# Kernel tuning notes

Hardware: AMD Instinct MI355X
Metric: run time of the kernel (lower is better)

The kernel has to match this reference:

```python
import jax, jax.numpy as jnp
import numpy as np

D_MODEL = 1024
N_HEADS = 16
HEAD = D_MODEL // N_HEADS
SEQ_THRESHOLD = 2048
EPS = 1e-12  # torch F.normalize eps


def setup_inputs() -> dict:
    key = jax.random.key(0)
    ks = jax.random.split(key, 12)
    B, L = 2, 2048
    s = 1.0 / np.sqrt(D_MODEL)
    inp = {
        "query": jax.random.normal(ks[0], (B, L, D_MODEL), jnp.float32),
        "key": jax.random.normal(ks[1], (B, L, D_MODEL), jnp.float32),
        "value": jax.random.normal(ks[2], (B, L, D_MODEL), jnp.float32),
        "mask": jnp.ones((B, 1, 1, L), jnp.int32),
        "Wq": jax.random.normal(ks[3], (D_MODEL, D_MODEL), jnp.float32) * s,
        "bq": jnp.zeros((D_MODEL,), jnp.float32),
        "Wk": jax.random.normal(ks[4], (D_MODEL, D_MODEL), jnp.float32) * s,
        "bk": jnp.zeros((D_MODEL,), jnp.float32),
        "Wv": jax.random.normal(ks[5], (D_MODEL, D_MODEL), jnp.float32) * s,
        "bv": jnp.zeros((D_MODEL,), jnp.float32),
        "Wo": jax.random.normal(ks[6], (D_MODEL, D_MODEL), jnp.float32) * s,
        "bo": jnp.zeros((D_MODEL,), jnp.float32),
        "scale": jnp.asarray(np.log2(SEQ_THRESHOLD**2 - SEQ_THRESHOLD), jnp.float32),
    }
    return inp


def _split_heads(x):  # [B,L,D] -> [B,H,L,hd]
    B, L, _ = x.shape
    return x.reshape(B, L, N_HEADS, HEAD).transpose(0, 2, 1, 3)


def _l2norm(x):
    n = jnp.sqrt(jnp.sum(x * x, axis=-1, keepdims=True))
    return x / jnp.maximum(n, EPS)


def reference(query, key, value, mask, Wq, bq, Wk, bk, Wv, bv, Wo, bo, scale):
    Q = _split_heads(query @ Wq.T + bq)
    K = _split_heads(key @ Wk.T + bk)
    V = _split_heads(value @ Wv.T + bv)
    Q = _l2norm(Q)
    K = _l2norm(K)
    # scaled cosine attention scores [B,H,Lq,Lk]
    scores = scale * jnp.einsum("bhqd,bhkd->bhqk", Q, K)
    scores = jnp.where(mask == 0, jnp.float32(-1e18), scores)
    attn = jax.nn.softmax(scores, axis=-1)
    ctx = jnp.einsum("bhqk,bhkd->bhqd", attn, V)
    B, H, Lq, hd = ctx.shape
    ctx = ctx.transpose(0, 2, 1, 3).reshape(B, Lq, H * hd)
    out = ctx @ Wo.T + bo
    return (out, attn)
```

## Files before the change

### kernel.cpp

```cpp
#include <hip/hip_runtime.h>
#include <hip/hip_bf16.h>
#include <stdint.h>

typedef __attribute__((ext_vector_type(8))) short bf16x8;
typedef __attribute__((ext_vector_type(4))) float f32x4;

#define LSEQ 2048
#define DM 1024
#define NH 16
#define HD 64

__device__ __forceinline__ unsigned short bf16r(float f) {
  unsigned u = __builtin_bit_cast(unsigned, f);
  u = (u + 0x7FFFu + ((u >> 16) & 1u)) >> 16;
  return (unsigned short)u;
}
__device__ __forceinline__ float bf16f(unsigned short h) {
  unsigned u = ((unsigned)h) << 16;
  return __builtin_bit_cast(float, u);
}

__device__ __forceinline__ void async16(const void* g, void* l) {
  __builtin_amdgcn_global_load_lds(
      (const __attribute__((address_space(1))) unsigned int*)g,
      (__attribute__((address_space(3))) unsigned int*)l, 16, 0, 0);
}

template <int ROWB>
__device__ __forceinline__ bf16x8 lds_frag_swz(const unsigned short* base, int row, int colbyte) {
  int addr = row * ROWB + colbyte;
  addr ^= ((row & 7) << 4);
  return *(const bf16x8*)((const char*)base + addr);
}
__device__ __forceinline__ void lds_store16_swz(unsigned short* base, int row, int col,
                                                unsigned short v) {
  int addr = row * 256 + col * 2;
  addr ^= ((row & 7) << 4);
  *(unsigned short*)((char*)base + addr) = v;
}

__global__ __launch_bounds__(256) void cvt3(const float* __restrict__ s0,
                                            const float* __restrict__ s1,
                                            const float* __restrict__ s2,
                                            unsigned short* __restrict__ d0,
                                            unsigned short* __restrict__ d1,
                                            unsigned short* __restrict__ d2, int n8) {
  int y = blockIdx.y;
  const float* s = (y == 0) ? s0 : (y == 1) ? s1 : s2;
  unsigned short* d = (y == 0) ? d0 : (y == 1) ? d1 : d2;
  int i = blockIdx.x * 256 + threadIdx.x;
  if (i >= n8) return;
  const float4* sp = (const float4*)s;
  float4 a = sp[2 * i], b = sp[2 * i + 1];
  union { unsigned short u[8]; uint4 v; } r;
  r.u[0] = bf16r(a.x); r.u[1] = bf16r(a.y); r.u[2] = bf16r(a.z); r.u[3] = bf16r(a.w);
  r.u[4] = bf16r(b.x); r.u[5] = bf16r(b.y); r.u[6] = bf16r(b.z); r.u[7] = bf16r(b.w);
  ((uint4*)d)[i] = r.v;
}
__global__ __launch_bounds__(256) void cvt4(const float* __restrict__ s0,
                                            const float* __restrict__ s1,
                                            const float* __restrict__ s2,
                                            const float* __restrict__ s3,
                                            unsigned short* __restrict__ d0,
                                            unsigned short* __restrict__ d1,
                                            unsigned short* __restrict__ d2,
                                            unsigned short* __restrict__ d3, int n8) {
  int y = blockIdx.y;
  const float* s = (y == 0) ? s0 : (y == 1) ? s1 : (y == 2) ? s2 : s3;
  unsigned short* d = (y == 0) ? d0 : (y == 1) ? d1 : (y == 2) ? d2 : d3;
  int i = blockIdx.x * 256 + threadIdx.x;
  if (i >= n8) return;
  const float4* sp = (const float4*)s;
  float4 a = sp[2 * i], b = sp[2 * i + 1];
  union { unsigned short u[8]; uint4 v; } r;
  r.u[0] = bf16r(a.x); r.u[1] = bf16r(a.y); r.u[2] = bf16r(a.z); r.u[3] = bf16r(a.w);
  r.u[4] = bf16r(b.x); r.u[5] = bf16r(b.y); r.u[6] = bf16r(b.z); r.u[7] = bf16r(b.w);
  ((uint4*)d)[i] = r.v;
}

__device__ __forceinline__ void gemm_core(const unsigned short* __restrict__ A,
                                          const unsigned short* __restrict__ Bw,
                                          const float* __restrict__ bias,
                                          void* __restrict__ Cout, int mode,
                                          unsigned short* As, unsigned short* Bs) {
  const int t = threadIdx.x, lane = t & 63, wid = t >> 6;
  const int mt = blockIdx.x, nt = blockIdx.y;
  const int wm = (wid >> 1) * 64, wn = (wid & 1) * 64;
  const int lq = lane >> 4, lr = lane & 15;

  f32x4 acc[4][4];
#pragma unroll
  for (int i = 0; i < 4; ++i)
#pragma unroll
    for (int j = 0; j < 4; ++j) acc[i][j] = (f32x4){0.f, 0.f, 0.f, 0.f};

  auto stage = [&](int k0) {
#pragma unroll
    for (int i = 0; i < 4; ++i) {
      int chunk = i * 256 + t;
      int row = chunk >> 3, j = chunk & 7;
      int sj = j ^ (row & 7);
      async16(A + (size_t)(mt * 128 + row) * DM + k0 + sj * 8, (char*)As + chunk * 16);
    }
#pragma unroll
    for (int i = 0; i < 4; ++i) {
      int chunk = i * 256 + t;
      int row = chunk >> 3, j = chunk & 7;
      int sj = j ^ (row & 7);
      async16(Bw + (size_t)(nt * 128 + row) * DM + k0 + sj * 8, (char*)Bs + chunk * 16);
    }
  };

  stage(0);
  for (int kt = 0; kt < DM / 64; ++kt) {
    __syncthreads();
    bf16x8 af[4][2], bfr[4][2];
#pragma unroll
    for (int mf = 0; mf < 4; ++mf) {
      int row = wm + mf * 16 + lr;
#pragma unroll
      for (int ks = 0; ks < 2; ++ks)
        af[mf][ks] = lds_frag_swz<128>(As, row, ks * 64 + lq * 16);
    }
#pragma unroll
    for (int nf = 0; nf < 4; ++nf) {
      int row = wn + nf * 16 + lr;
#pragma unroll
      for (int ks = 0; ks < 2; ++ks)
        bfr[nf][ks] = lds_frag_swz<128>(Bs, row, ks * 64 + lq * 16);
    }
    __syncthreads();
    if (kt + 1 < DM / 64) stage((kt + 1) * 64);
#pragma unroll
    for (int ks = 0; ks < 2; ++ks)
#pragma unroll
      for (int mf = 0; mf < 4; ++mf)
#pragma unroll
        for (int nf = 0; nf < 4; ++nf)
          acc[mf][nf] = __builtin_amdgcn_mfma_f32_16x16x32_bf16(af[mf][ks], bfr[nf][ks],
                                                                acc[mf][nf], 0, 0, 0);
  }

  const int gn0 = nt * 128 + wn;
  float bv[4];
#pragma unroll
  for (int nf = 0; nf < 4; ++nf) bv[nf] = bias[gn0 + nf * 16 + lr];
#pragma unroll
  for (int mf = 0; mf < 4; ++mf) {
    float v[4][4];
#pragma unroll
    for (int nf = 0; nf < 4; ++nf)
#pragma unroll
      for (int r = 0; r < 4; ++r) v[nf][r] = acc[mf][nf][r] + bv[nf];
    if (mode == 1) {
#pragma unroll
      for (int r = 0; r < 4; ++r) {
        float ss = v[0][r] * v[0][r] + v[1][r] * v[1][r] + v[2][r] * v[2][r] + v[3][r] * v[3][r];
        ss += __shfl_xor(ss, 1, 64);
        ss += __shfl_xor(ss, 2, 64);
        ss += __shfl_xor(ss, 4, 64);
        ss += __shfl_xor(ss, 8, 64);
        float rn = 1.0f / fmaxf(sqrtf(ss), 1e-12f);
#pragma unroll
        for (int nf = 0; nf < 4; ++nf) v[nf][r] *= rn;
      }
    }
    const int gm0 = mt * 128 + wm + mf * 16 + lq * 4;
    if (mode == 2) {
      float* C = (float*)Cout;
#pragma unroll
      for (int r = 0; r < 4; ++r)
#pragma unroll
        for (int nf = 0; nf < 4; ++nf)
          C[(size_t)(gm0 + r) * DM + gn0 + nf * 16 + lr] = v[nf][r];
    } else {
      unsigned short* C = (unsigned short*)Cout;
#pragma unroll
      for (int r = 0; r < 4; ++r)
#pragma unroll
        for (int nf = 0; nf < 4; ++nf)
          C[(size_t)(gm0 + r) * DM + gn0 + nf * 16 + lr] = bf16r(v[nf][r]);
    }
  }
}

__global__ __launch_bounds__(256) void gemm_qkv(
    const unsigned short* __restrict__ A0, const unsigned short* __restrict__ A1,
    const unsigned short* __restrict__ A2, const unsigned short* __restrict__ W0,
    const unsigned short* __restrict__ W1, const unsigned short* __restrict__ W2,
    const float* __restrict__ b0, const float* __restrict__ b1, const float* __restrict__ b2,
    unsigned short* __restrict__ C0, unsigned short* __restrict__ C1,
    unsigned short* __restrict__ C2) {
  __shared__ unsigned short As[128 * 64];
  __shared__ unsigned short Bs[128 * 64];
  int z = blockIdx.z;
  const unsigned short* A = (z == 0) ? A0 : (z == 1) ? A1 : A2;
  const unsigned short* W = (z == 0) ? W0 : (z == 1) ? W1 : W2;
  const float* bias = (z == 0) ? b0 : (z == 1) ? b1 : b2;
  unsigned short* C = (z == 0) ? C0 : (z == 1) ? C1 : C2;
  gemm_core(A, W, bias, C, (z == 2) ? 0 : 1, As, Bs);
}

__global__ __launch_bounds__(256) void gemm_o(const unsigned short* __restrict__ A,
                                              const unsigned short* __restrict__ W,
                                              const float* __restrict__ bias,
                                              float* __restrict__ C) {
  __shared__ unsigned short As[128 * 64];
  __shared__ unsigned short Bs[128 * 64];
  gemm_core(A, W, bias, C, 2, As, Bs);
}

__global__ __launch_bounds__(256) void transpose_v(const unsigned short* __restrict__ V,
                                                   unsigned short* __restrict__ Vt) {
  __shared__ unsigned short T[64][72];
  const int lt = blockIdx.x, h = blockIdx.y, b = blockIdx.z;
  const int t = threadIdx.x;
  const int r = t >> 2, c0 = (t & 3) * 16;
  const unsigned short* g = V + ((size_t)(b * LSEQ + lt * 64 + r) * DM + h * 64 + c0);
  *(uint4*)&T[r][c0] = *(const uint4*)g;
  *(uint4*)&T[r][c0 + 8] = *(const uint4*)(g + 8);
  __syncthreads();
  const int d = t >> 2, l0 = (t & 3) * 16;
  union { unsigned short u[16]; uint4 v[2]; } o;
#pragma unroll
  for (int j = 0; j < 16; ++j) o.u[j] = T[l0 + j][d];
  unsigned short* og = Vt + ((size_t)((b * NH + h) * HD + d) * LSEQ + lt * 64 + l0);
  ((uint4*)og)[0] = o.v[0];
  ((uint4*)og)[1] = o.v[1];
}

__global__ __launch_bounds__(256) void attn_kernel(
    const unsigned short* __restrict__ Qn, const unsigned short* __restrict__ Kn,
    const unsigned short* __restrict__ Vt, const int* __restrict__ mask,
    const float* __restrict__ scale_p, float* __restrict__ attn_out,
    unsigned short* __restrict__ ctx) {
  __shared__ unsigned short PQs[64 * 128];
  __shared__ unsigned short Ks[128 * 64];
  __shared__ unsigned short Vs[64 * 128];
  const int qt = blockIdx.x, h = blockIdx.y, b = blockIdx.z;
  const int t = threadIdx.x, lane = t & 63, wid = t >> 6;
  const int lq = lane >> 4, lr = lane & 15;
  const int wq = wid * 16;
  const float k2 = scale_p[0] * 1.4426950408889634f;

  const unsigned short* Qg = Qn + ((size_t)(b * LSEQ + qt * 64) * DM + h * HD);
  const unsigned short* Kg = Kn + ((size_t)b * LSEQ * DM + h * HD);
  const unsigned short* Vg = Vt + (size_t)(b * NH + h) * HD * LSEQ;
  float* attn_g = attn_out + ((size_t)((b * NH + h) * LSEQ + qt * 64)) * LSEQ;
  const int* mg = mask + b * LSEQ;

  auto stageK = [&](int k0) {
#pragma unroll
    for (int i = 0; i < 4; ++i) {
      int chunk = i * 256 + t;
      int row = chunk >> 3, j = chunk & 7;
      async16(Kg + (size_t)(k0 + row) * DM + (j ^ (row & 7)) * 8, (char*)Ks + chunk * 16);
    }
  };
  auto stageV = [&](int k0) {
#pragma unroll
    for (int i = 0; i < 4; ++i) {
      int chunk = i * 256 + t;
      int row = chunk >> 4, j = chunk & 15;
      async16(Vg + (size_t)row * LSEQ + k0 + (j ^ (row & 7)) * 8, (char*)Vs + chunk * 16);
    }
  };

#pragma unroll
  for (int i = 0; i < 2; ++i) {
    int chunk = i * 256 + t;
    int row = chunk >> 3, j = chunk & 7;
    async16(Qg + (size_t)row * DM + (j ^ (row & 7)) * 8, (char*)PQs + chunk * 16);
  }
  stageK(0);

  bf16x8 qa[2];
  float rsum[4] = {0.f, 0.f, 0.f, 0.f};

  auto qk_tile = [&](f32x4 (&c)[8]) {
#pragma unroll
    for (int nf = 0; nf < 8; ++nf) {
      int row = nf * 16 + lr;
      bf16x8 k0f = lds_frag_swz<128>(Ks, row, lq * 16);
      bf16x8 k1f = lds_frag_swz<128>(Ks, row, 64 + lq * 16);
      f32x4 z = (f32x4){0.f, 0.f, 0.f, 0.f};
      z = __builtin_amdgcn_mfma_f32_16x16x32_bf16(qa[0], k0f, z, 0, 0, 0);
      z = __builtin_amdgcn_mfma_f32_16x16x32_bf16(qa[1], k1f, z, 0, 0, 0);
      c[nf] = z;
    }
  };

  for (int kt = 0; kt < LSEQ / 128; ++kt) {
    __syncthreads();
    if (kt == 0) {
      int row = wq + lr;
      qa[0] = lds_frag_swz<128>(PQs, row, lq * 16);
      qa[1] = lds_frag_swz<128>(PQs, row, 64 + lq * 16);
    }
    f32x4 c[8];
    qk_tile(c);
    __syncthreads();
    if (kt + 1 < LSEQ / 128) stageK((kt + 1) * 128);
#pragma unroll
    for (int nf = 0; nf < 8; ++nf) {
      int mv = mg[kt * 128 + nf * 16 + lr];
#pragma unroll
      for (int r = 0; r < 4; ++r) {
        float p = exp2f(c[nf][r] * k2);
        rsum[r] += mv ? p : 0.f;
      }
    }
  }
  stageK(0);
  stageV(0);
#pragma unroll
  for (int off = 1; off < 16; off <<= 1)
#pragma unroll
    for (int r = 0; r < 4; ++r) rsum[r] += __shfl_xor(rsum[r], off, 64);
  float sinv[4];
#pragma unroll
  for (int r = 0; r < 4; ++r) sinv[r] = 1.0f / fmaxf(rsum[r], 1e-30f);

  f32x4 opv[4];
#pragma unroll
  for (int nf = 0; nf < 4; ++nf) opv[nf] = (f32x4){0.f, 0.f, 0.f, 0.f};
  unsigned short* Ps = PQs;
  for (int kt = 0; kt < LSEQ / 128; ++kt) {
    __syncthreads();
    f32x4 c[8];
    qk_tile(c);
#pragma unroll
    for (int nf = 0; nf < 8; ++nf) {
      int mv = mg[kt * 128 + nf * 16 + lr];
#pragma unroll
      for (int r = 0; r < 4; ++r) {
        float p = mv ? exp2f(c[nf][r] * k2) * sinv[r] : 0.f;
        lds_store16_swz(Ps, wq + lq * 4 + r, nf * 16 + lr, bf16r(p));
      }
    }
    __syncthreads();
    if (kt + 1 < LSEQ / 128) stageK((kt + 1) * 128);
    {
      int rr = t >> 4, c8 = (t & 15) * 8;
      float* og = attn_g + kt * 128 + c8;
#pragma unroll
      for (int gi = 0; gi < 4; ++gi) {
        int row = gi * 16 + rr;
        bf16x8 p8 = lds_frag_swz<256>(Ps, row, c8 * 2);
        f32x4 f0, f1;
        f0[0] = bf16f((unsigned short)p8[0]); f0[1] = bf16f((unsigned short)p8[1]);
        f0[2] = bf16f((unsigned short)p8[2]); f0[3] = bf16f((unsigned short)p8[3]);
        f1[0] = bf16f((unsigned short)p8[4]); f1[1] = bf16f((unsigned short)p8[5]);
        f1[2] = bf16f((unsigned short)p8[6]); f1[3] = bf16f((unsigned short)p8[7]);
        float* rp = og + (size_t)row * LSEQ;
        __builtin_nontemporal_store(f0, (f32x4*)rp);
        __builtin_nontemporal_store(f1, (f32x4*)(rp + 4));
      }
    }
#pragma unroll
    for (int ks = 0; ks < 4; ++ks) {
      bf16x8 pa = lds_frag_swz<256>(Ps, wq + lr, ks * 64 + lq * 16);
#pragma unroll
      for (int nf = 0; nf < 4; ++nf) {
        bf16x8 vb = lds_frag_swz<256>(Vs, nf * 16 + lr, ks * 64 + lq * 16);
        opv[nf] = __builtin_amdgcn_mfma_f32_16x16x32_bf16(pa, vb, opv[nf], 0, 0, 0);
      }
    }
    __syncthreads();
    if (kt + 1 < LSEQ / 128) stageV((kt + 1) * 128);
  }
#pragma unroll
  for (int nf = 0; nf < 4; ++nf)
#pragma unroll
    for (int r = 0; r < 4; ++r) {
      int q = wq + lq * 4 + r;
      int d = nf * 16 + lr;
      ctx[(size_t)(b * LSEQ + qt * 64 + q) * DM + h * HD + d] = bf16r(opv[nf][r]);
    }
}

extern "C" void kernel_launch(void* const* d_in, const int* in_sizes, int n_in,
                              void* d_out, int out_size, void* d_ws, size_t ws_size,
                              hipStream_t stream) {
  const float* query = (const float*)d_in[0];
  const float* key_ = (const float*)d_in[1];
  const float* value = (const float*)d_in[2];
  const int* mask = (const int*)d_in[3];
  const float* Wq = (const float*)d_in[4];
  const float* bq = (const float*)d_in[5];
  const float* Wk = (const float*)d_in[6];
  const float* bk = (const float*)d_in[7];
  const float* Wv = (const float*)d_in[8];
  const float* bv = (const float*)d_in[9];
  const float* Wo = (const float*)d_in[10];
  const float* bo = (const float*)d_in[11];
  const float* scale = (const float*)d_in[12];

  char* ws = (char*)d_ws;
  const size_t XB = 8388608;
  const size_t WB = 2097152;
  unsigned short* qb = (unsigned short*)(ws);
  unsigned short* kb = (unsigned short*)(ws + XB);
  unsigned short* vb = (unsigned short*)(ws + 2 * XB);
  unsigned short* wqb = (unsigned short*)(ws + 3 * XB);
  unsigned short* wkb = (unsigned short*)(ws + 3 * XB + WB);
  unsigned short* wvb = (unsigned short*)(ws + 3 * XB + 2 * WB);
  unsigned short* wob = (unsigned short*)(ws + 3 * XB + 3 * WB);
  unsigned short* Qnb = (unsigned short*)(ws + 3 * XB + 4 * WB);
  unsigned short* Knb = (unsigned short*)(ws + 4 * XB + 4 * WB);
  unsigned short* Vb = (unsigned short*)(ws + 5 * XB + 4 * WB);
  unsigned short* Vtb = (unsigned short*)(ws + 6 * XB + 4 * WB);
  unsigned short* ctxb = (unsigned short*)(ws + 7 * XB + 4 * WB);

  cvt3<<<dim3(2048, 3), 256, 0, stream>>>(query, key_, value, qb, kb, vb, 524288);
  cvt4<<<dim3(512, 4), 256, 0, stream>>>(Wq, Wk, Wv, Wo, wqb, wkb, wvb, wob, 131072);

  gemm_qkv<<<dim3(32, 8, 3), 256, 0, stream>>>(qb, kb, vb, wqb, wkb, wvb, bq, bk, bv,
                                               Qnb, Knb, Vb);
  transpose_v<<<dim3(32, NH, 2), 256, 0, stream>>>(Vb, Vtb);

  float* attn_out = (float*)d_out + 4194304;
  attn_kernel<<<dim3(32, NH, 2), 256, 0, stream>>>(Qnb, Knb, Vtb, mask, scale, attn_out, ctxb);

  gemm_o<<<dim3(32, 8), 256, 0, stream>>>(ctxb, wob, bo, (float*)d_out);
}
```

Baseline: 291.6 us.

## Fuse V transpose into QKV GEMM and keep attention probabilities in registers

The V projection GEMM now writes its output directly in transposed per-head layout, which removes the separate transpose kernel and its buffer. The attention kernel computes S^T with swapped MFMA operands. Probabilities are stored to the attn output straight from registers and packed to bf16 with v_cvt_pk_bf16, then redistributed through cross-lane shuffles into the PV MFMA operand, so the LDS round-trip for P is gone. The mask is preloaded to LDS as bf16 multipliers, the K/V staging sync is merged, and launch bounds allow 4 blocks per CU. The costs are extra shuffle instructions and strided 8-byte stores in the V epilogue.

```diff
diff --git a/kernel.cpp b/kernel.cpp
--- a/kernel.cpp
+++ b/kernel.cpp
@@ -19,6 +19,11 @@
   unsigned u = ((unsigned)h) << 16;
   return __builtin_bit_cast(float, u);
 }
+__device__ __forceinline__ unsigned cvt_pk_bf16(float a, float b) {
+  unsigned r;
+  asm("v_cvt_pk_bf16_f32 %0, %1, %2" : "=v"(r) : "v"(a), "v"(b));
+  return r;
+}
 
 __device__ __forceinline__ void async16(const void* g, void* l) {
   __builtin_amdgcn_global_load_lds(
@@ -26,17 +31,15 @@
       (__attribute__((address_space(3))) unsigned int*)l, 16, 0, 0);
 }
 
-template <int ROWB>
 __device__ __forceinline__ bf16x8 lds_frag_swz(const unsigned short* base, int row, int colbyte) {
-  int addr = row * ROWB + colbyte;
+  int addr = row * 128 + colbyte;
   addr ^= ((row & 7) << 4);
   return *(const bf16x8*)((const char*)base + addr);
 }
-__device__ __forceinline__ void lds_store16_swz(unsigned short* base, int row, int col,
-                                                unsigned short v) {
-  int addr = row * 256 + col * 2;
-  addr ^= ((row & 7) << 4);
-  *(unsigned short*)((char*)base + addr) = v;
+__device__ __forceinline__ bf16x8 lds_frag_swzV(const unsigned short* base, int row, int colbyte) {
+  int addr = row * 256 + colbyte;
+  addr ^= ((row & 15) << 4);
+  return *(const bf16x8*)((const char*)base + addr);
 }
 
 __global__ __launch_bounds__(256) void cvt3(const float* __restrict__ s0,
@@ -78,10 +81,11 @@
   ((uint4*)d)[i] = r.v;
 }
 
+template <int MODE>
 __device__ __forceinline__ void gemm_core(const unsigned short* __restrict__ A,
                                           const unsigned short* __restrict__ Bw,
                                           const float* __restrict__ bias,
-                                          void* __restrict__ Cout, int mode,
+                                          void* __restrict__ Cout,
                                           unsigned short* As, unsigned short* Bs) {
   const int t = threadIdx.x, lane = t & 63, wid = t >> 6;
   const int mt = blockIdx.x, nt = blockIdx.y;
@@ -120,14 +124,14 @@
       int row = wm + mf * 16 + lr;
 #pragma unroll
       for (int ks = 0; ks < 2; ++ks)
-        af[mf][ks] = lds_frag_swz<128>(As, row, ks * 64 + lq * 16);
+        af[mf][ks] = lds_frag_swz(As, row, ks * 64 + lq * 16);
     }
 #pragma unroll
     for (int nf = 0; nf < 4; ++nf) {
       int row = wn + nf * 16 + lr;
 #pragma unroll
       for (int ks = 0; ks < 2; ++ks)
-        bfr[nf][ks] = lds_frag_swz<128>(Bs, row, ks * 64 + lq * 16);
+        bfr[nf][ks] = lds_frag_swz(Bs, row, ks * 64 + lq * 16);
     }
     __syncthreads();
     if (kt + 1 < DM / 64) stage((kt + 1) * 64);
@@ -152,7 +156,7 @@
     for (int nf = 0; nf < 4; ++nf)
 #pragma unroll
       for (int r = 0; r < 4; ++r) v[nf][r] = acc[mf][nf][r] + bv[nf];
-    if (mode == 1) {
+    if (MODE == 1) {
 #pragma unroll
       for (int r = 0; r < 4; ++r) {
         float ss = v[0][r] * v[0][r] + v[1][r] * v[1][r] + v[2][r] * v[2][r] + v[3][r] * v[3][r];
@@ -166,13 +170,25 @@
       }
     }
     const int gm0 = mt * 128 + wm + mf * 16 + lq * 4;
-    if (mode == 2) {
+    if (MODE == 2) {
       float* C = (float*)Cout;
 #pragma unroll
       for (int r = 0; r < 4; ++r)
 #pragma unroll
         for (int nf = 0; nf < 4; ++nf)
           C[(size_t)(gm0 + r) * DM + gn0 + nf * 16 + lr] = v[nf][r];
+    } else if (MODE == 3) {
+      unsigned short* Vt = (unsigned short*)Cout;
+      const int bb = gm0 >> 11, ll = gm0 & 2047;
+#pragma unroll
+      for (int nf = 0; nf < 4; ++nf) {
+        int col = gn0 + nf * 16 + lr;
+        int hh = col >> 6, dd = col & 63;
+        ushort4 o;
+        o.x = bf16r(v[nf][0]); o.y = bf16r(v[nf][1]);
+        o.z = bf16r(v[nf][2]); o.w = bf16r(v[nf][3]);
+        *(ushort4*)&Vt[(size_t)((bb * NH + hh) * HD + dd) * LSEQ + ll] = o;
+      }
     } else {
       unsigned short* C = (unsigned short*)Cout;
 #pragma unroll
@@ -194,11 +210,9 @@
   __shared__ unsigned short As[128 * 64];
   __shared__ unsigned short Bs[128 * 64];
   int z = blockIdx.z;
-  const unsigned short* A = (z == 0) ? A0 : (z == 1) ? A1 : A2;
-  const unsigned short* W = (z == 0) ? W0 : (z == 1) ? W1 : W2;
-  const float* bias = (z == 0) ? b0 : (z == 1) ? b1 : b2;
-  unsigned short* C = (z == 0) ? C0 : (z == 1) ? C1 : C2;
-  gemm_core(A, W, bias, C, (z == 2) ? 0 : 1, As, Bs);
+  if (z == 0) gemm_core<1>(A0, W0, b0, C0, As, Bs);
+  else if (z == 1) gemm_core<1>(A1, W1, b1, C1, As, Bs);
+  else gemm_core<3>(A2, W2, b2, C2, As, Bs);
 }
 
 __global__ __launch_bounds__(256) void gemm_o(const unsigned short* __restrict__ A,
@@ -207,36 +221,17 @@
                                               float* __restrict__ C) {
   __shared__ unsigned short As[128 * 64];
   __shared__ unsigned short Bs[128 * 64];
-  gemm_core(A, W, bias, C, 2, As, Bs);
-}
-
-__global__ __launch_bounds__(256) void transpose_v(const unsigned short* __restrict__ V,
-                                                   unsigned short* __restrict__ Vt) {
-  __shared__ unsigned short T[64][72];
-  const int lt = blockIdx.x, h = blockIdx.y, b = blockIdx.z;
-  const int t = threadIdx.x;
-  const int r = t >> 2, c0 = (t & 3) * 16;
-  const unsigned short* g = V + ((size_t)(b * LSEQ + lt * 64 + r) * DM + h * 64 + c0);
-  *(uint4*)&T[r][c0] = *(const uint4*)g;
-  *(uint4*)&T[r][c0 + 8] = *(const uint4*)(g + 8);
-  __syncthreads();
-  const int d = t >> 2, l0 = (t & 3) * 16;
-  union { unsigned short u[16]; uint4 v[2]; } o;
-#pragma unroll
-  for (int j = 0; j < 16; ++j) o.u[j] = T[l0 + j][d];
-  unsigned short* og = Vt + ((size_t)((b * NH + h) * HD + d) * LSEQ + lt * 64 + l0);
-  ((uint4*)og)[0] = o.v[0];
-  ((uint4*)og)[1] = o.v[1];
-}
-
-__global__ __launch_bounds__(256) void attn_kernel(
+  gemm_core<2>(A, W, bias, C, As, Bs);
+}
+
+__global__ __launch_bounds__(256, 4) void attn_kernel(
     const unsigned short* __restrict__ Qn, const unsigned short* __restrict__ Kn,
     const unsigned short* __restrict__ Vt, const int* __restrict__ mask,
     const float* __restrict__ scale_p, float* __restrict__ attn_out,
     unsigned short* __restrict__ ctx) {
-  __shared__ unsigned short PQs[64 * 128];
+  __shared__ unsigned short QVs[64 * 128];
   __shared__ unsigned short Ks[128 * 64];
-  __shared__ unsigned short Vs[64 * 128];
+  __shared__ unsigned short Ms[2048];
   const int qt = blockIdx.x, h = blockIdx.y, b = blockIdx.z;
   const int t = threadIdx.x, lane = t & 63, wid = t >> 6;
   const int lq = lane >> 4, lr = lane & 15;
@@ -262,121 +257,115 @@
     for (int i = 0; i < 4; ++i) {
       int chunk = i * 256 + t;
       int row = chunk >> 4, j = chunk & 15;
-      async16(Vg + (size_t)row * LSEQ + k0 + (j ^ (row & 7)) * 8, (char*)Vs + chunk * 16);
+      async16(Vg + (size_t)row * LSEQ + k0 + (j ^ (row & 15)) * 8, (char*)QVs + chunk * 16);
     }
   };
 
+  {
+    const int4* mp = (const int4*)mg;
+    int4 m0 = mp[t * 2], m1 = mp[t * 2 + 1];
+    union { unsigned short u[8]; uint4 v; } mo;
+    mo.u[0] = m0.x ? 0x3F80 : 0; mo.u[1] = m0.y ? 0x3F80 : 0;
+    mo.u[2] = m0.z ? 0x3F80 : 0; mo.u[3] = m0.w ? 0x3F80 : 0;
+    mo.u[4] = m1.x ? 0x3F80 : 0; mo.u[5] = m1.y ? 0x3F80 : 0;
+    mo.u[6] = m1.z ? 0x3F80 : 0; mo.u[7] = m1.w ? 0x3F80 : 0;
+    ((uint4*)Ms)[t] = mo.v;
+  }
 #pragma unroll
   for (int i = 0; i < 2; ++i) {
     int chunk = i * 256 + t;
     int row = chunk >> 3, j = chunk & 7;
-    async16(Qg + (size_t)row * DM + (j ^ (row & 7)) * 8, (char*)PQs + chunk * 16);
+    async16(Qg + (size_t)row * DM + (j ^ (row & 7)) * 8, (char*)QVs + chunk * 16);
   }
   stageK(0);
 
   bf16x8 qa[2];
-  float rsum[4] = {0.f, 0.f, 0.f, 0.f};
-
-  auto qk_tile = [&](f32x4 (&c)[8]) {
+  float rsum = 0.f;
+
+  for (int kt = 0; kt < LSEQ / 128; ++kt) {
+    __syncthreads();
+    if (kt == 0) {
+      qa[0] = lds_frag_swz(QVs, wq + lr, lq * 16);
+      qa[1] = lds_frag_swz(QVs, wq + lr, 64 + lq * 16);
+    }
 #pragma unroll
     for (int nf = 0; nf < 8; ++nf) {
-      int row = nf * 16 + lr;
-      bf16x8 k0f = lds_frag_swz<128>(Ks, row, lq * 16);
-      bf16x8 k1f = lds_frag_swz<128>(Ks, row, 64 + lq * 16);
+      bf16x8 k0f = lds_frag_swz(Ks, nf * 16 + lr, lq * 16);
+      bf16x8 k1f = lds_frag_swz(Ks, nf * 16 + lr, 64 + lq * 16);
       f32x4 z = (f32x4){0.f, 0.f, 0.f, 0.f};
-      z = __builtin_amdgcn_mfma_f32_16x16x32_bf16(qa[0], k0f, z, 0, 0, 0);
-      z = __builtin_amdgcn_mfma_f32_16x16x32_bf16(qa[1], k1f, z, 0, 0, 0);
-      c[nf] = z;
-    }
-  };
-
-  for (int kt = 0; kt < LSEQ / 128; ++kt) {
-    __syncthreads();
-    if (kt == 0) {
-      int row = wq + lr;
-      qa[0] = lds_frag_swz<128>(PQs, row, lq * 16);
-      qa[1] = lds_frag_swz<128>(PQs, row, 64 + lq * 16);
-    }
-    f32x4 c[8];
-    qk_tile(c);
+      z = __builtin_amdgcn_mfma_f32_16x16x32_bf16(k0f, qa[0], z, 0, 0, 0);
+      z = __builtin_amdgcn_mfma_f32_16x16x32_bf16(k1f, qa[1], z, 0, 0, 0);
+      ushort4 m4 = *(const ushort4*)&Ms[kt * 128 + nf * 16 + lq * 4];
+      rsum += exp2f(z[0] * k2) * bf16f(m4.x);
+      rsum += exp2f(z[1] * k2) * bf16f(m4.y);
+      rsum += exp2f(z[2] * k2) * bf16f(m4.z);
+      rsum += exp2f(z[3] * k2) * bf16f(m4.w);
+    }
     __syncthreads();
     if (kt + 1 < LSEQ / 128) stageK((kt + 1) * 128);
-#pragma unroll
-    for (int nf = 0; nf < 8; ++nf) {
-      int mv = mg[kt * 128 + nf * 16 + lr];
-#pragma unroll
-      for (int r = 0; r < 4; ++r) {
-        float p = exp2f(c[nf][r] * k2);
-        rsum[r] += mv ? p : 0.f;
-      }
-    }
-  }
+  }
+  rsum += __shfl_xor(rsum, 16, 64);
+  rsum += __shfl_xor(rsum, 32, 64);
+  const float sinv = 1.0f / fmaxf(rsum, 1e-30f);
+
   stageK(0);
   stageV(0);
-#pragma unroll
-  for (int off = 1; off < 16; off <<= 1)
-#pragma unroll
-    for (int r = 0; r < 4; ++r) rsum[r] += __shfl_xor(rsum[r], off, 64);
-  float sinv[4];
-#pragma unroll
-  for (int r = 0; r < 4; ++r) sinv[r] = 1.0f / fmaxf(rsum[r], 1e-30f);
-
   f32x4 opv[4];
 #pragma unroll
   for (int nf = 0; nf < 4; ++nf) opv[nf] = (f32x4){0.f, 0.f, 0.f, 0.f};
-  unsigned short* Ps = PQs;
+  const int s0 = (lq & 1) * 32 + lr, s1 = s0 + 16;
+  const bool hi = (lq >> 1) != 0;
+
   for (int kt = 0; kt < LSEQ / 128; ++kt) {
     __syncthreads();
-    f32x4 c[8];
-    qk_tile(c);
+    unsigned pw[16];
 #pragma unroll
     for (int nf = 0; nf < 8; ++nf) {
-      int mv = mg[kt * 128 + nf * 16 + lr];
-#pragma unroll
-      for (int r = 0; r < 4; ++r) {
-        float p = mv ? exp2f(c[nf][r] * k2) * sinv[r] : 0.f;
-        lds_store16_swz(Ps, wq + lq * 4 + r, nf * 16 + lr, bf16r(p));
+      bf16x8 k0f = lds_frag_swz(Ks, nf * 16 + lr, lq * 16);
+      bf16x8 k1f = lds_frag_swz(Ks, nf * 16 + lr, 64 + lq * 16);
+      f32x4 z = (f32x4){0.f, 0.f, 0.f, 0.f};
+      z = __builtin_amdgcn_mfma_f32_16x16x32_bf16(k0f, qa[0], z, 0, 0, 0);
+      z = __builtin_amdgcn_mfma_f32_16x16x32_bf16(k1f, qa[1], z, 0, 0, 0);
+      ushort4 m4 = *(const ushort4*)&Ms[kt * 128 + nf * 16 + lq * 4];
+      float p0 = exp2f(z[0] * k2) * bf16f(m4.x) * sinv;
+      float p1 = exp2f(z[1] * k2) * bf16f(m4.y) * sinv;
+      float p2 = exp2f(z[2] * k2) * bf16f(m4.z) * sinv;
+      float p3 = exp2f(z[3] * k2) * bf16f(m4.w) * sinv;
+      f32x4 st = (f32x4){p0, p1, p2, p3};
+      __builtin_nontemporal_store(
+          st, (f32x4*)(attn_g + (size_t)(wq + lr) * LSEQ + kt * 128 + nf * 16 + lq * 4));
+      pw[nf * 2] = cvt_pk_bf16(p0, p1);
+      pw[nf * 2 + 1] = cvt_pk_bf16(p2, p3);
+    }
+#pragma unroll
+    for (int ks = 0; ks < 4; ++ks) {
+      unsigned a0 = pw[4 * ks], a1 = pw[4 * ks + 1];
+      unsigned b0 = pw[4 * ks + 2], b1 = pw[4 * ks + 3];
+      unsigned ua0 = __shfl((int)a0, s0, 64), ua1 = __shfl((int)a1, s0, 64);
+      unsigned ua2 = __shfl((int)a0, s1, 64), ua3 = __shfl((int)a1, s1, 64);
+      unsigned ub0 = __shfl((int)b0, s0, 64), ub1 = __shfl((int)b1, s0, 64);
+      unsigned ub2 = __shfl((int)b0, s1, 64), ub3 = __shfl((int)b1, s1, 64);
+      union { unsigned w[4]; bf16x8 v; } pf;
+      pf.w[0] = hi ? ub0 : ua0;
+      pf.w[1] = hi ? ub1 : ua1;
+      pf.w[2] = hi ? ub2 : ua2;
+      pf.w[3] = hi ? ub3 : ua3;
+#pragma unroll
+      for (int nf = 0; nf < 4; ++nf) {
+        bf16x8 vb = lds_frag_swzV(QVs, nf * 16 + lr, ks * 64 + lq * 16);
+        opv[nf] = __builtin_amdgcn_mfma_f32_16x16x32_bf16(vb, pf.v, opv[nf], 0, 0, 0);
       }
     }
     __syncthreads();
-    if (kt + 1 < LSEQ / 128) stageK((kt + 1) * 128);
-    {
-      int rr = t >> 4, c8 = (t & 15) * 8;
-      float* og = attn_g + kt * 128 + c8;
-#pragma unroll
-      for (int gi = 0; gi < 4; ++gi) {
-        int row = gi * 16 + rr;
-        bf16x8 p8 = lds_frag_swz<256>(Ps, row, c8 * 2);
-        f32x4 f0, f1;
-        f0[0] = bf16f((unsigned short)p8[0]); f0[1] = bf16f((unsigned short)p8[1]);
-        f0[2] = bf16f((unsigned short)p8[2]); f0[3] = bf16f((unsigned short)p8[3]);
-        f1[0] = bf16f((unsigned short)p8[4]); f1[1] = bf16f((unsigned short)p8[5]);
-        f1[2] = bf16f((unsigned short)p8[6]); f1[3] = bf16f((unsigned short)p8[7]);
-        float* rp = og + (size_t)row * LSEQ;
-        __builtin_nontemporal_store(f0, (f32x4*)rp);
-        __builtin_nontemporal_store(f1, (f32x4*)(rp + 4));
-      }
-    }
-#pragma unroll
-    for (int ks = 0; ks < 4; ++ks) {
-      bf16x8 pa = lds_frag_swz<256>(Ps, wq + lr, ks * 64 + lq * 16);
-#pragma unroll
-      for (int nf = 0; nf < 4; ++nf) {
-        bf16x8 vb = lds_frag_swz<256>(Vs, nf * 16 + lr, ks * 64 + lq * 16);
-        opv[nf] = __builtin_amdgcn_mfma_f32_16x16x32_bf16(pa, vb, opv[nf], 0, 0, 0);
-      }
-    }
-    __syncthreads();
-    if (kt + 1 < LSEQ / 128) stageV((kt + 1) * 128);
-  }
-#pragma unroll
-  for (int nf = 0; nf < 4; ++nf)
-#pragma unroll
-    for (int r = 0; r < 4; ++r) {
-      int q = wq + lq * 4 + r;
-      int d = nf * 16 + lr;
-      ctx[(size_t)(b * LSEQ + qt * 64 + q) * DM + h * HD + d] = bf16r(opv[nf][r]);
-    }
+    if (kt + 1 < LSEQ / 128) { stageK((kt + 1) * 128); stageV((kt + 1) * 128); }
+  }
+#pragma unroll
+  for (int nf = 0; nf < 4; ++nf) {
+    ushort4 o;
+    o.x = bf16r(opv[nf][0]); o.y = bf16r(opv[nf][1]);
+    o.z = bf16r(opv[nf][2]); o.w = bf16r(opv[nf][3]);
+    *(ushort4*)&ctx[(size_t)(b * LSEQ + qt * 64 + wq + lr) * DM + h * HD + nf * 16 + lq * 4] = o;
+  }
 }
 
 extern "C" void kernel_launch(void* const* d_in, const int* in_sizes, int n_in,
@@ -408,16 +397,14 @@
   unsigned short* wob = (unsigned short*)(ws + 3 * XB + 3 * WB);
   unsigned short* Qnb = (unsigned short*)(ws + 3 * XB + 4 * WB);
   unsigned short* Knb = (unsigned short*)(ws + 4 * XB + 4 * WB);
-  unsigned short* Vb = (unsigned short*)(ws + 5 * XB + 4 * WB);
-  unsigned short* Vtb = (unsigned short*)(ws + 6 * XB + 4 * WB);
-  unsigned short* ctxb = (unsigned short*)(ws + 7 * XB + 4 * WB);
+  unsigned short* Vtb = (unsigned short*)(ws + 5 * XB + 4 * WB);
+  unsigned short* ctxb = (unsigned short*)(ws + 6 * XB + 4 * WB);
 
   cvt3<<<dim3(2048, 3), 256, 0, stream>>>(query, key_, value, qb, kb, vb, 524288);
   cvt4<<<dim3(512, 4), 256, 0, stream>>>(Wq, Wk, Wv, Wo, wqb, wkb, wvb, wob, 131072);
 
   gemm_qkv<<<dim3(32, 8, 3), 256, 0, stream>>>(qb, kb, vb, wqb, wkb, wvb, bq, bk, bv,
-                                               Qnb, Knb, Vb);
-  transpose_v<<<dim3(32, NH, 2), 256, 0, stream>>>(Vb, Vtb);
+                                               Qnb, Knb, Vtb);
 
   float* attn_out = (float*)d_out + 4194304;
   attn_kernel<<<dim3(32, NH, 2), 256, 0, stream>>>(Qnb, Knb, Vtb, mask, scale, attn_out, ctxb);
```

New measurement: 287.9 us. Within noise of the previous version (-1.3%).
